# Kernel optimization log

Measured on AMD Instinct MI355X. Metric: run time of the kernel, lower is better.

The kernel has to match this reference:

```python
import jax, jax.numpy as jnp
import numpy as np

N = 50000      # nodes
E = 800000     # edges (avg degree 16)
F_IN = 512     # input features
H = 64         # hidden
C = 40         # classes
L = 4          # FAConv layers
EPS = 0.2      # args.epsilon


def setup_inputs() -> dict:
    key = jax.random.key(0)
    ks = jax.random.split(key, 8)
    gain = 1.414
    x = jax.random.normal(ks[0], (N, F_IN), jnp.float32)
    edge_index = jax.random.randint(ks[1], (2, E), 0, N, dtype=jnp.int32)
    W1 = jax.random.normal(ks[2], (H, F_IN), jnp.float32) * (gain * np.sqrt(2.0 / (F_IN + H)))
    b1 = jnp.zeros((H,), jnp.float32)
    W2 = jax.random.normal(ks[3], (C, H), jnp.float32) * (gain * np.sqrt(2.0 / (H + C)))
    b2 = jnp.zeros((C,), jnp.float32)
    att_l = jax.random.normal(ks[4], (L, H), jnp.float32) * np.sqrt(2.0 / (1 + H))
    att_r = jax.random.normal(ks[5], (L, H), jnp.float32) * np.sqrt(2.0 / (1 + H))
    return {"x": x, "edge_index": edge_index, "W1": W1, "b1": b1,
            "W2": W2, "b2": b2, "att_l": att_l, "att_r": att_r}


def reference(x, edge_index, W1, b1, W2, b2, att_l, att_r):
    n = x.shape[0]
    src, dst = edge_index[0], edge_index[1]
    # gcn_norm with self-loops (FAConv normalize=True, add_self_loops=True)
    loop = jnp.arange(n, dtype=src.dtype)
    rows = jnp.concatenate([src, loop])  # source j
    cols = jnp.concatenate([dst, loop])  # target i
    deg = jax.ops.segment_sum(jnp.ones_like(cols, dtype=x.dtype), cols, num_segments=n)
    dinv = jnp.where(deg > 0, jax.lax.rsqrt(jnp.maximum(deg, 1e-12)), 0.0)
    norm = dinv[rows] * dinv[cols]  # [E+N]

    # lin1 + relu (dropout inactive in eval)
    h = jax.nn.relu(x @ W1.T + b1)
    raw = h
    for l in range(L):
        al = h @ att_l[l]  # [N] per-source score
        ar = h @ att_r[l]  # [N] per-target score
        a = jnp.tanh(al[rows] + ar[cols])          # [E+N]
        msg = h[rows] * (a * norm)[:, None]        # [E+N, H]
        h = jax.ops.segment_sum(msg, cols, num_segments=n) + EPS * raw
    logits = h @ W2.T + b2
    return jax.nn.log_softmax(logits, axis=1)
```

## Files before the change

### kernel.cpp

```cpp
#include <hip/hip_runtime.h>

#define F_IN 512
#define HDIM 64
#define NCLS 40
#define NLAYER 4
#define EPS_F 0.2f

typedef __attribute__((ext_vector_type(8))) short short8;
typedef __attribute__((ext_vector_type(4))) float f32x4;
typedef __attribute__((ext_vector_type(8))) unsigned short ushort8;
typedef unsigned long long u64;

__device__ __forceinline__ unsigned short f2bf(float f) {
  unsigned u = __float_as_uint(f);
  u += 0x7FFFu + ((u >> 16) & 1u);
  return (unsigned short)(u >> 16);
}
__device__ __forceinline__ float bf2f(unsigned short s) {
  return __uint_as_float(((unsigned)s) << 16);
}

__global__ __launch_bounds__(256) void k_init(int* indeg, int nN) {
  int i = blockIdx.x * 256 + threadIdx.x;
  if (i < nN) indeg[i] = 0;
}

__global__ __launch_bounds__(256) void k_hist(const int* __restrict__ dst, int* indeg,
                                              int* __restrict__ rank, int nE) {
  int e = blockIdx.x * 256 + threadIdx.x;
  if (e < nE) rank[e] = atomicAdd(&indeg[dst[e]], 1);
}

__global__ __launch_bounds__(256) void k_bsum(const int* __restrict__ indeg, int* bsum, int nN) {
  int i0 = blockIdx.x * 512 + threadIdx.x;
  int v = 0;
  if (i0 < nN) v += indeg[i0];
  if (i0 + 256 < nN) v += indeg[i0 + 256];
#pragma unroll
  for (int off = 32; off > 0; off >>= 1) v += __shfl_xor(v, off, 64);
  __shared__ int s[4];
  if ((threadIdx.x & 63) == 0) s[threadIdx.x >> 6] = v;
  __syncthreads();
  if (threadIdx.x == 0) bsum[blockIdx.x] = s[0] + s[1] + s[2] + s[3];
}

__global__ __launch_bounds__(128) void k_bscan(const int* __restrict__ bsum, int* bpre,
                                               int* rowptr, int nblk, int nN, int nE) {
  __shared__ int sb[128];
  int t = threadIdx.x;
  int v = (t < nblk) ? bsum[t] : 0;
  sb[t] = v;
  __syncthreads();
  int acc = v;
  for (int off = 1; off < 128; off <<= 1) {
    int o = (t >= off) ? sb[t - off] : 0;
    __syncthreads();
    acc += o;
    sb[t] = acc;
    __syncthreads();
  }
  if (t < nblk) bpre[t] = acc - v;
  if (t == 0) rowptr[nN] = nE;
}

__global__ __launch_bounds__(512) void k_rowptr(const int* __restrict__ indeg,
                                                const int* __restrict__ bpre,
                                                const float* __restrict__ al,
                                                const float* __restrict__ ar,
                                                int* rowptr,
                                                float2* P, float2* Q, float* selfc, int nN) {
  __shared__ int sb[512];
  int t = threadIdx.x;
  int i = blockIdx.x * 512 + t;
  int v = (i < nN) ? indeg[i] : 0;
  sb[t] = v;
  __syncthreads();
  int acc = v;
  for (int off = 1; off < 512; off <<= 1) {
    int o = (t >= off) ? sb[t - off] : 0;
    __syncthreads();
    acc += o;
    sb[t] = acc;
    __syncthreads();
  }
  if (i < nN) {
    rowptr[i] = bpre[blockIdx.x] + acc - v;
    float dv = rsqrtf((float)v + 1.0f);
    float a = al[i], r = ar[i];
    P[i] = make_float2(a, dv);
    Q[i] = make_float2(r, dv);
    selfc[i] = tanhf(a + r) * dv * dv;
  }
}

__global__ __launch_bounds__(256) void k_scatter(const int* __restrict__ src,
                                                 const int* __restrict__ dst,
                                                 const int* __restrict__ rank,
                                                 const int* __restrict__ rowptr,
                                                 int* __restrict__ csrsrc, int nE) {
  int e = blockIdx.x * 256 + threadIdx.x;
  if (e < nE) {
    int d = dst[e];
    csrsrc[rowptr[d] + rank[e]] = src[e];
  }
}

__global__ __launch_bounds__(256) void k_lin1(const float* __restrict__ x,
                                              const float* __restrict__ W1,
                                              const float* __restrict__ b1,
                                              const float* __restrict__ attl0,
                                              const float* __restrict__ attr0,
                                              unsigned short* __restrict__ hraw,
                                              float* __restrict__ al, float* __restrict__ ar,
                                              int nN) {
  __shared__ unsigned short xs[64 * 64];
  __shared__ unsigned short ws[64 * 64];
  const int t = threadIdx.x;
  const int wv = t >> 6;
  const int l = t & 63;
  const int n0 = blockIdx.x * 64;
  const int srow = t >> 2;
  const int sk4 = (t & 3) * 4;
  const bool xvalid = (n0 + srow) < nN;
  const f32x4* x4 = reinterpret_cast<const f32x4*>(x);
  const f32x4* w4 = reinterpret_cast<const f32x4*>(W1);
  short8* xs8 = reinterpret_cast<short8*>(xs);
  short8* ws8 = reinterpret_cast<short8*>(ws);
  const int wslot0 = srow * 8 + (((t & 3) * 2 + 0) ^ (srow & 7));
  const int wslot1 = srow * 8 + (((t & 3) * 2 + 1) ^ (srow & 7));
  const int arow = l & 15;
  const int kgrp = l >> 4;
  f32x4 acc[4] = {{0.f, 0.f, 0.f, 0.f},
                  {0.f, 0.f, 0.f, 0.f},
                  {0.f, 0.f, 0.f, 0.f},
                  {0.f, 0.f, 0.f, 0.f}};
  f32x4 xa[4], wa[4];
  const f32x4 zero4 = {0.f, 0.f, 0.f, 0.f};
  {
    const size_t xb = (size_t)(n0 + srow) * (F_IN / 4) + sk4;
    const size_t wb = (size_t)srow * (F_IN / 4) + sk4;
#pragma unroll
    for (int r = 0; r < 4; ++r) {
      xa[r] = xvalid ? x4[xb + r] : zero4;
      wa[r] = w4[wb + r];
    }
  }
  for (int c = 0; c < 8; ++c) {
    short8 p0, p1, q0, q1;
#pragma unroll
    for (int r = 0; r < 2; ++r) {
#pragma unroll
      for (int j = 0; j < 4; ++j) {
        p0[r * 4 + j] = (short)f2bf(xa[r][j]);
        p1[r * 4 + j] = (short)f2bf(xa[2 + r][j]);
        q0[r * 4 + j] = (short)f2bf(wa[r][j]);
        q1[r * 4 + j] = (short)f2bf(wa[2 + r][j]);
      }
    }
    xs8[wslot0] = p0;
    xs8[wslot1] = p1;
    ws8[wslot0] = q0;
    ws8[wslot1] = q1;
    __syncthreads();
    if (c < 7) {
      const size_t xb = (size_t)(n0 + srow) * (F_IN / 4) + (c + 1) * 16 + sk4;
      const size_t wb = (size_t)srow * (F_IN / 4) + (c + 1) * 16 + sk4;
#pragma unroll
      for (int r = 0; r < 4; ++r) {
        xa[r] = xvalid ? x4[xb + r] : zero4;
        wa[r] = w4[wb + r];
      }
    }
#pragma unroll
    for (int c2 = 0; c2 < 2; ++c2) {
      const short8 a = xs8[(wv * 16 + arow) * 8 + ((c2 * 4 + kgrp) ^ (arow & 7))];
#pragma unroll
      for (int fs = 0; fs < 4; ++fs) {
        const short8 b = ws8[(fs * 16 + arow) * 8 + ((c2 * 4 + kgrp) ^ (arow & 7))];
        acc[fs] = __builtin_amdgcn_mfma_f32_16x16x32_bf16(a, b, acc[fs], 0, 0, 0);
      }
    }
    __syncthreads();
  }
  float psl[4] = {0.f, 0.f, 0.f, 0.f};
  float psr[4] = {0.f, 0.f, 0.f, 0.f};
#pragma unroll
  for (int fs = 0; fs < 4; ++fs) {
    const int feat = fs * 16 + arow;
    const float bias = b1[feat];
    const float atl = attl0[feat];
    const float atr = attr0[feat];
#pragma unroll
    for (int j = 0; j < 4; ++j) {
      const float v = fmaxf(acc[fs][j] + bias, 0.f);
      const int node = n0 + wv * 16 + kgrp * 4 + j;
      if (node < nN) hraw[(size_t)node * HDIM + feat] = f2bf(v);
      psl[j] = fmaf(v, atl, psl[j]);
      psr[j] = fmaf(v, atr, psr[j]);
    }
  }
#pragma unroll
  for (int off = 1; off <= 8; off <<= 1) {
#pragma unroll
    for (int j = 0; j < 4; ++j) {
      psl[j] += __shfl_xor(psl[j], off, 64);
      psr[j] += __shfl_xor(psr[j], off, 64);
    }
  }
  if (arow == 0) {
#pragma unroll
    for (int j = 0; j < 4; ++j) {
      const int node = n0 + wv * 16 + kgrp * 4 + j;
      if (node < nN) {
        al[node] = psl[j];
        ar[node] = psr[j];
      }
    }
  }
}

template <bool WNEXT>
__global__ __launch_bounds__(256) void k_agg(const unsigned short* __restrict__ h,
                                             const unsigned short* __restrict__ hraw,
                                             const int* __restrict__ rowptr,
                                             const int* __restrict__ csrsrc,
                                             const float2* __restrict__ Pc,
                                             const float2* __restrict__ Qc,
                                             const float* __restrict__ Sc,
                                             const float* __restrict__ attl_n,
                                             const float* __restrict__ attr_n,
                                             float2* __restrict__ Pn, float2* __restrict__ Qn,
                                             float* __restrict__ Sn,
                                             unsigned short* __restrict__ hout, int nN) {
  const int wid = threadIdx.x >> 6, lane = threadIdx.x & 63;
  const int d = blockIdx.x * 4 + wid;
  if (d >= nN) return;
  const int grp = lane >> 3;
  const int fo = (lane & 7) * 8;
  const size_t base = (size_t)d * HDIM + fo;
  const float2 qd = Qc[d];
  float acc[8] = {};
  if (grp == 0) {
    const float sc = Sc[d];
    const ushort8 hd = *reinterpret_cast<const ushort8*>(&h[base]);
    const ushort8 rw = *reinterpret_cast<const ushort8*>(&hraw[base]);
#pragma unroll
    for (int j = 0; j < 8; ++j) acc[j] = fmaf(bf2f(hd[j]), sc, EPS_F * bf2f(rw[j]));
  }
  const int e1 = rowptr[d + 1];
  int e = rowptr[d] + grp;
  for (; e + 8 < e1; e += 16) {
    const int s0 = csrsrc[e];
    const int s1 = csrsrc[e + 8];
    const float2 p0 = Pc[s0];
    const float2 p1 = Pc[s1];
    const ushort8 h0v = *reinterpret_cast<const ushort8*>(&h[(size_t)s0 * HDIM + fo]);
    const ushort8 h1v = *reinterpret_cast<const ushort8*>(&h[(size_t)s1 * HDIM + fo]);
    const float c0 = tanhf(p0.x + qd.x) * (p0.y * qd.y);
    const float c1 = tanhf(p1.x + qd.x) * (p1.y * qd.y);
#pragma unroll
    for (int j = 0; j < 8; ++j) acc[j] = fmaf(bf2f(h0v[j]), c0, acc[j]);
#pragma unroll
    for (int j = 0; j < 8; ++j) acc[j] = fmaf(bf2f(h1v[j]), c1, acc[j]);
  }
  for (; e < e1; e += 8) {
    const int s = csrsrc[e];
    const float2 p = Pc[s];
    const ushort8 hv = *reinterpret_cast<const ushort8*>(&h[(size_t)s * HDIM + fo]);
    const float c = tanhf(p.x + qd.x) * (p.y * qd.y);
#pragma unroll
    for (int j = 0; j < 8; ++j) acc[j] = fmaf(bf2f(hv[j]), c, acc[j]);
  }
#pragma unroll
  for (int off = 8; off <= 32; off <<= 1) {
#pragma unroll
    for (int j = 0; j < 8; ++j) acc[j] += __shfl_xor(acc[j], off, 64);
  }
  if (grp == 0) {
    ushort8 o;
#pragma unroll
    for (int j = 0; j < 8; ++j) o[j] = f2bf(acc[j]);
    *reinterpret_cast<ushort8*>(&hout[base]) = o;
  }
  if (WNEXT) {
    float psl = 0.f, psr = 0.f;
#pragma unroll
    for (int j = 0; j < 8; ++j) {
      psl = fmaf(acc[j], attl_n[fo + j], psl);
      psr = fmaf(acc[j], attr_n[fo + j], psr);
    }
#pragma unroll
    for (int off = 1; off <= 4; off <<= 1) {
      psl += __shfl_xor(psl, off, 64);
      psr += __shfl_xor(psr, off, 64);
    }
    if (lane == 0) {
      Pn[d] = make_float2(psl, qd.y);
      Qn[d] = make_float2(psr, qd.y);
      Sn[d] = tanhf(psl + psr) * qd.y * qd.y;
    }
  }
}

__global__ __launch_bounds__(256) void k_out(const unsigned short* __restrict__ h,
                                             const float* __restrict__ W2,
                                             const float* __restrict__ b2,
                                             float* __restrict__ out, int nN) {
  __shared__ float w2s[NCLS * HDIM];
  __shared__ float b2s[NCLS];
  for (int i = threadIdx.x; i < NCLS * HDIM; i += 256) w2s[i] = W2[i];
  if (threadIdx.x < NCLS) b2s[threadIdx.x] = b2[threadIdx.x];
  __syncthreads();
  const int n = blockIdx.x * 256 + threadIdx.x;
  if (n >= nN) return;
  float hr[HDIM];
  const ushort8* hrow = reinterpret_cast<const ushort8*>(&h[(size_t)n * HDIM]);
#pragma unroll
  for (int r = 0; r < 8; ++r) {
    const ushort8 v = hrow[r];
#pragma unroll
    for (int j = 0; j < 8; ++j) hr[r * 8 + j] = bf2f(v[j]);
  }
  const float4* w2s4 = reinterpret_cast<const float4*>(w2s);
  float logits[NCLS];
  float m = -INFINITY;
#pragma unroll
  for (int c = 0; c < NCLS; ++c) {
    float a0 = 0.f, a1 = 0.f, a2 = 0.f, a3 = 0.f;
#pragma unroll
    for (int j4 = 0; j4 < HDIM / 4; j4 += 4) {
      const float4 w0 = w2s4[c * (HDIM / 4) + j4 + 0];
      const float4 w1 = w2s4[c * (HDIM / 4) + j4 + 1];
      const float4 w2v = w2s4[c * (HDIM / 4) + j4 + 2];
      const float4 w3 = w2s4[c * (HDIM / 4) + j4 + 3];
      const int j = j4 * 4;
      a0 = fmaf(hr[j + 0], w0.x, a0);  a0 = fmaf(hr[j + 1], w0.y, a0);
      a0 = fmaf(hr[j + 2], w0.z, a0);  a0 = fmaf(hr[j + 3], w0.w, a0);
      a1 = fmaf(hr[j + 4], w1.x, a1);  a1 = fmaf(hr[j + 5], w1.y, a1);
      a1 = fmaf(hr[j + 6], w1.z, a1);  a1 = fmaf(hr[j + 7], w1.w, a1);
      a2 = fmaf(hr[j + 8], w2v.x, a2); a2 = fmaf(hr[j + 9], w2v.y, a2);
      a2 = fmaf(hr[j + 10], w2v.z, a2); a2 = fmaf(hr[j + 11], w2v.w, a2);
      a3 = fmaf(hr[j + 12], w3.x, a3); a3 = fmaf(hr[j + 13], w3.y, a3);
      a3 = fmaf(hr[j + 14], w3.z, a3); a3 = fmaf(hr[j + 15], w3.w, a3);
    }
    const float lg = (a0 + a1) + (a2 + a3) + b2s[c];
    logits[c] = lg;
    m = fmaxf(m, lg);
  }
  float s = 0.f;
#pragma unroll
  for (int c = 0; c < NCLS; ++c) s += expf(logits[c] - m);
  const float lse = m + logf(s);
  float4* o4 = reinterpret_cast<float4*>(&out[(size_t)n * NCLS]);
#pragma unroll
  for (int c4 = 0; c4 < NCLS / 4; ++c4) {
    float4 o;
    o.x = logits[c4 * 4 + 0] - lse;
    o.y = logits[c4 * 4 + 1] - lse;
    o.z = logits[c4 * 4 + 2] - lse;
    o.w = logits[c4 * 4 + 3] - lse;
    o4[c4] = o;
  }
}

extern "C" void kernel_launch(void* const* d_in, const int* in_sizes, int n_in,
                              void* d_out, int out_size, void* d_ws, size_t ws_size,
                              hipStream_t stream) {
  const float* x = (const float*)d_in[0];
  const int* ei = (const int*)d_in[1];
  const float* W1 = (const float*)d_in[2];
  const float* b1 = (const float*)d_in[3];
  const float* W2 = (const float*)d_in[4];
  const float* b2 = (const float*)d_in[5];
  const float* attl = (const float*)d_in[6];
  const float* attr = (const float*)d_in[7];
  float* out = (float*)d_out;

  const int nN = in_sizes[0] / F_IN;
  const int nE = in_sizes[1] / 2;
  const int* src = ei;
  const int* dst = ei + nE;

  char* w = (char*)d_ws;
  size_t off = 0;
  auto alloc = [&](size_t bytes) {
    void* p = (void*)(w + off);
    off = (off + bytes + 255) & ~(size_t)255;
    return p;
  };
  unsigned short* hraw = (unsigned short*)alloc((size_t)nN * HDIM * 2);
  unsigned short* hA = (unsigned short*)alloc((size_t)nN * HDIM * 2);
  unsigned short* hB = (unsigned short*)alloc((size_t)nN * HDIM * 2);
  float2* P0 = (float2*)alloc((size_t)nN * 8);
  float2* Q0 = (float2*)alloc((size_t)nN * 8);
  float* S0 = (float*)alloc((size_t)nN * 4);
  float2* P1 = (float2*)alloc((size_t)nN * 8);
  float2* Q1 = (float2*)alloc((size_t)nN * 8);
  float* S1 = (float*)alloc((size_t)nN * 4);
  float* al = (float*)alloc((size_t)nN * 4);
  float* ar = (float*)alloc((size_t)nN * 4);
  int* indeg = (int*)alloc((size_t)nN * 4);
  int* rank = (int*)alloc((size_t)nE * 4);
  int* rowptr = (int*)alloc((size_t)(nN + 1) * 4);
  int* csrsrc = (int*)alloc((size_t)nE * 4);
  int* bsum = (int*)alloc(1024);
  int* bpre = (int*)alloc(1024);

  const int nb_n = (nN + 255) / 256;
  const int nb_e = (nE + 255) / 256;
  const int nblk = (nN + 511) / 512;
  const int nb4 = (nN + 3) / 4;

  k_lin1<<<(nN + 63) / 64, 256, 0, stream>>>(x, W1, b1, attl, attr, hraw, al, ar, nN);
  k_init<<<nb_n, 256, 0, stream>>>(indeg, nN);
  k_hist<<<nb_e, 256, 0, stream>>>(dst, indeg, rank, nE);
  k_bsum<<<nblk, 256, 0, stream>>>(indeg, bsum, nN);
  k_bscan<<<1, 128, 0, stream>>>(bsum, bpre, rowptr, nblk, nN, nE);
  k_rowptr<<<nblk, 512, 0, stream>>>(indeg, bpre, al, ar, rowptr, P0, Q0, S0, nN);
  k_scatter<<<nb_e, 256, 0, stream>>>(src, dst, rank, rowptr, csrsrc, nE);

  const unsigned short* hin = hraw;
  unsigned short* hout = hA;
  float2 *Pc = P0, *Qc = Q0, *Pn = P1, *Qn = Q1;
  float *Sc = S0, *Sn = S1;
  for (int l = 0; l < NLAYER; ++l) {
    if (l < NLAYER - 1) {
      k_agg<true><<<nb4, 256, 0, stream>>>(hin, hraw, rowptr, csrsrc, Pc, Qc, Sc,
                                           attl + (l + 1) * HDIM, attr + (l + 1) * HDIM,
                                           Pn, Qn, Sn, hout, nN);
    } else {
      k_agg<false><<<nb4, 256, 0, stream>>>(hin, hraw, rowptr, csrsrc, Pc, Qc, Sc,
                                            nullptr, nullptr, Pn, Qn, Sn, hout, nN);
    }
    hin = hout;
    hout = (hout == hA) ? hB : hA;
    float2* tp = Pc; Pc = Pn; Pn = tp;
    float2* tq = Qc; Qc = Qn; Qn = tq;
    float* ts = Sc; Sc = Sn; Sn = ts;
  }
  k_out<<<nb_n, 256, 0, stream>>>(hin, W2, b2, out, nN);
}
```

Measured before the change: 238.2 us.

## Process two destination nodes per wavefront in aggregation and use fast tanh

```diff
diff --git a/kernel.cpp b/kernel.cpp
--- a/kernel.cpp
+++ b/kernel.cpp
@@ -18,6 +18,10 @@
 }
 __device__ __forceinline__ float bf2f(unsigned short s) {
   return __uint_as_float(((unsigned)s) << 16);
+}
+__device__ __forceinline__ float ftanh(float x) {
+  float e = __expf(2.0f * x);
+  return fmaf(-2.0f, __builtin_amdgcn_rcpf(e + 1.0f), 1.0f);
 }
 
 __global__ __launch_bounds__(256) void k_init(int* indeg, int nN) {
@@ -233,71 +237,99 @@
                                              float* __restrict__ Sn,
                                              unsigned short* __restrict__ hout, int nN) {
   const int wid = threadIdx.x >> 6, lane = threadIdx.x & 63;
-  const int d = blockIdx.x * 4 + wid;
-  if (d >= nN) return;
+  const int dA = blockIdx.x * 8 + wid * 2;
+  if (dA >= nN) return;
+  const int dB = dA + 1;
+  const bool hasB = dB < nN;
+  const int dBs = hasB ? dB : dA;
   const int grp = lane >> 3;
   const int fo = (lane & 7) * 8;
-  const size_t base = (size_t)d * HDIM + fo;
-  const float2 qd = Qc[d];
-  float acc[8] = {};
+  const size_t baseA = (size_t)dA * HDIM + fo;
+  const size_t baseB = (size_t)dBs * HDIM + fo;
+  const float2 qdA = Qc[dA];
+  const float2 qdB = Qc[dBs];
+  float accA[8] = {}, accB[8] = {};
   if (grp == 0) {
-    const float sc = Sc[d];
-    const ushort8 hd = *reinterpret_cast<const ushort8*>(&h[base]);
-    const ushort8 rw = *reinterpret_cast<const ushort8*>(&hraw[base]);
-#pragma unroll
-    for (int j = 0; j < 8; ++j) acc[j] = fmaf(bf2f(hd[j]), sc, EPS_F * bf2f(rw[j]));
-  }
-  const int e1 = rowptr[d + 1];
-  int e = rowptr[d] + grp;
-  for (; e + 8 < e1; e += 16) {
-    const int s0 = csrsrc[e];
-    const int s1 = csrsrc[e + 8];
-    const float2 p0 = Pc[s0];
-    const float2 p1 = Pc[s1];
-    const ushort8 h0v = *reinterpret_cast<const ushort8*>(&h[(size_t)s0 * HDIM + fo]);
-    const ushort8 h1v = *reinterpret_cast<const ushort8*>(&h[(size_t)s1 * HDIM + fo]);
-    const float c0 = tanhf(p0.x + qd.x) * (p0.y * qd.y);
-    const float c1 = tanhf(p1.x + qd.x) * (p1.y * qd.y);
-#pragma unroll
-    for (int j = 0; j < 8; ++j) acc[j] = fmaf(bf2f(h0v[j]), c0, acc[j]);
-#pragma unroll
-    for (int j = 0; j < 8; ++j) acc[j] = fmaf(bf2f(h1v[j]), c1, acc[j]);
-  }
-  for (; e < e1; e += 8) {
-    const int s = csrsrc[e];
-    const float2 p = Pc[s];
-    const ushort8 hv = *reinterpret_cast<const ushort8*>(&h[(size_t)s * HDIM + fo]);
-    const float c = tanhf(p.x + qd.x) * (p.y * qd.y);
-#pragma unroll
-    for (int j = 0; j < 8; ++j) acc[j] = fmaf(bf2f(hv[j]), c, acc[j]);
+    const float sc = Sc[dA];
+    const ushort8 hd = *reinterpret_cast<const ushort8*>(&h[baseA]);
+    const ushort8 rw = *reinterpret_cast<const ushort8*>(&hraw[baseA]);
+#pragma unroll
+    for (int j = 0; j < 8; ++j) accA[j] = fmaf(bf2f(hd[j]), sc, EPS_F * bf2f(rw[j]));
+  } else if (grp == 1 && hasB) {
+    const float sc = Sc[dBs];
+    const ushort8 hd = *reinterpret_cast<const ushort8*>(&h[baseB]);
+    const ushort8 rw = *reinterpret_cast<const ushort8*>(&hraw[baseB]);
+#pragma unroll
+    for (int j = 0; j < 8; ++j) accB[j] = fmaf(bf2f(hd[j]), sc, EPS_F * bf2f(rw[j]));
+  }
+  const int r1A = rowptr[dA + 1];
+  const int r1B = rowptr[dBs + 1];
+  int eA = rowptr[dA] + grp;
+  int eB = hasB ? (rowptr[dBs] + grp) : r1B;
+  while (eA < r1A || eB < r1B) {
+    const bool vA = eA < r1A;
+    const bool vB = eB < r1B;
+    const int sA = csrsrc[vA ? eA : 0];
+    const int sB = csrsrc[vB ? eB : 0];
+    const float2 pA = Pc[sA];
+    const float2 pB = Pc[sB];
+    const ushort8 hA = *reinterpret_cast<const ushort8*>(&h[(size_t)sA * HDIM + fo]);
+    const ushort8 hB = *reinterpret_cast<const ushort8*>(&h[(size_t)sB * HDIM + fo]);
+    const float cA = vA ? ftanh(pA.x + qdA.x) * (pA.y * qdA.y) : 0.f;
+    const float cB = vB ? ftanh(pB.x + qdB.x) * (pB.y * qdB.y) : 0.f;
+#pragma unroll
+    for (int j = 0; j < 8; ++j) accA[j] = fmaf(bf2f(hA[j]), cA, accA[j]);
+#pragma unroll
+    for (int j = 0; j < 8; ++j) accB[j] = fmaf(bf2f(hB[j]), cB, accB[j]);
+    eA += 8;
+    eB += 8;
   }
 #pragma unroll
   for (int off = 8; off <= 32; off <<= 1) {
 #pragma unroll
-    for (int j = 0; j < 8; ++j) acc[j] += __shfl_xor(acc[j], off, 64);
+    for (int j = 0; j < 8; ++j) {
+      accA[j] += __shfl_xor(accA[j], off, 64);
+      accB[j] += __shfl_xor(accB[j], off, 64);
+    }
   }
   if (grp == 0) {
     ushort8 o;
 #pragma unroll
-    for (int j = 0; j < 8; ++j) o[j] = f2bf(acc[j]);
-    *reinterpret_cast<ushort8*>(&hout[base]) = o;
+    for (int j = 0; j < 8; ++j) o[j] = f2bf(accA[j]);
+    *reinterpret_cast<ushort8*>(&hout[baseA]) = o;
+  } else if (grp == 1 && hasB) {
+    ushort8 o;
+#pragma unroll
+    for (int j = 0; j < 8; ++j) o[j] = f2bf(accB[j]);
+    *reinterpret_cast<ushort8*>(&hout[baseB]) = o;
   }
   if (WNEXT) {
-    float psl = 0.f, psr = 0.f;
+    float pslA = 0.f, psrA = 0.f, pslB = 0.f, psrB = 0.f;
 #pragma unroll
     for (int j = 0; j < 8; ++j) {
-      psl = fmaf(acc[j], attl_n[fo + j], psl);
-      psr = fmaf(acc[j], attr_n[fo + j], psr);
+      const float wl = attl_n[fo + j];
+      const float wr = attr_n[fo + j];
+      pslA = fmaf(accA[j], wl, pslA);
+      psrA = fmaf(accA[j], wr, psrA);
+      pslB = fmaf(accB[j], wl, pslB);
+      psrB = fmaf(accB[j], wr, psrB);
     }
 #pragma unroll
     for (int off = 1; off <= 4; off <<= 1) {
-      psl += __shfl_xor(psl, off, 64);
-      psr += __shfl_xor(psr, off, 64);
+      pslA += __shfl_xor(pslA, off, 64);
+      psrA += __shfl_xor(psrA, off, 64);
+      pslB += __shfl_xor(pslB, off, 64);
+      psrB += __shfl_xor(psrB, off, 64);
     }
     if (lane == 0) {
-      Pn[d] = make_float2(psl, qd.y);
-      Qn[d] = make_float2(psr, qd.y);
-      Sn[d] = tanhf(psl + psr) * qd.y * qd.y;
+      Pn[dA] = make_float2(pslA, qdA.y);
+      Qn[dA] = make_float2(psrA, qdA.y);
+      Sn[dA] = ftanh(pslA + psrA) * qdA.y * qdA.y;
+      if (hasB) {
+        Pn[dB] = make_float2(pslB, qdB.y);
+        Qn[dB] = make_float2(psrB, qdB.y);
+        Sn[dB] = ftanh(pslB + psrB) * qdB.y * qdB.y;
+      }
     }
   }
 }
@@ -409,7 +441,7 @@
   const int nb_n = (nN + 255) / 256;
   const int nb_e = (nE + 255) / 256;
   const int nblk = (nN + 511) / 512;
-  const int nb4 = (nN + 3) / 4;
+  const int nb8 = (nN + 7) / 8;
 
   k_lin1<<<(nN + 63) / 64, 256, 0, stream>>>(x, W1, b1, attl, attr, hraw, al, ar, nN);
   k_init<<<nb_n, 256, 0, stream>>>(indeg, nN);
@@ -425,11 +457,11 @@
   float *Sc = S0, *Sn = S1;
   for (int l = 0; l < NLAYER; ++l) {
     if (l < NLAYER - 1) {
-      k_agg<true><<<nb4, 256, 0, stream>>>(hin, hraw, rowptr, csrsrc, Pc, Qc, Sc,
+      k_agg<true><<<nb8, 256, 0, stream>>>(hin, hraw, rowptr, csrsrc, Pc, Qc, Sc,
                                            attl + (l + 1) * HDIM, attr + (l + 1) * HDIM,
                                            Pn, Qn, Sn, hout, nN);
     } else {
-      k_agg<false><<<nb4, 256, 0, stream>>>(hin, hraw, rowptr, csrsrc, Pc, Qc, Sc,
+      k_agg<false><<<nb8, 256, 0, stream>>>(hin, hraw, rowptr, csrsrc, Pc, Qc, Sc,
                                             nullptr, nullptr, Pn, Qn, Sn, hout, nN);
     }
     hin = hout;
```

New measurement: 223.0 us. 1.07x faster.
